# Performance work log

Hardware: AMD Instinct MI355X
Metric: run time of the kernel (lower is better)

Reference implementation:

```python
import jax, jax.numpy as jnp
import numpy as np

H = 16
W = 16
THRESH = 1.0
B = 32

# NOTE: [5.0, 1.0] reproduces the (likely buggy) constant in the original source.
SRC_POINTS = jnp.array([[0.0,0.0],[0.5,0.0],[1.0,0.0],[0.0,0.5],[0.5,0.5],[1.0,0.5],[0.0,1.0],[5.0,1.0],[1.0,1.0]], dtype=jnp.float32)

def _conv(x, w, stride, padding):
    return jax.lax.conv_general_dilated(x, w, (stride, stride), padding, dimension_numbers=('NHWC', 'HWIO', 'NHWC'))

def _tps_u(r):
    return r * r * jnp.log(r + 1e-6)

def _pdist(a, b):
    # a [...,2], b [n,2] -> [..., n] euclidean distances (eps for sqrt-at-0 safety)
    return jnp.sqrt(jnp.sum((a[..., None, :] - b) ** 2, axis=-1) + 1e-12)

def _tps_fit(ctrl, values):
    # cheind/py-thin-plate-spline TPS.fit with reduced=True. ctrl [n,2], values [n] -> theta [n+2]
    n = ctrl.shape[0]
    K = _tps_u(_pdist(ctrl, ctrl))
    P = jnp.concatenate([jnp.ones((n, 1), ctrl.dtype), ctrl], axis=1)
    A = jnp.zeros((n + 3, n + 3), ctrl.dtype)
    A = A.at[:n, :n].set(K).at[:n, n:].set(P).at[n:, :n].set(P.T)
    v = jnp.zeros(n + 3, ctrl.dtype).at[:n].set(values)
    theta = jnp.linalg.solve(A, v)
    return theta[1:]

def _tps_z(pts, ctrl, theta):
    # pts [m,2], theta reduced [n+2] -> [m]
    U = _tps_u(_pdist(pts, ctrl))
    w, a = theta[:-3], theta[-3:]
    w = jnp.concatenate([-jnp.sum(w, keepdims=True), w])
    return U @ w + a[0] + pts[:, 0] * a[1] + pts[:, 1] * a[2]

def _inlier_mask(geo):
    # geo [18] -> mask [H, W, H, W], mask[a_y, a_x, b_y, b_x]
    mv = geo.reshape(9, 2)
    dst = SRC_POINTS + mv
    delta = SRC_POINTS - dst  # c_src - c_dst (tps_theta_from_points)
    th_x = _tps_fit(dst, delta[:, 0])
    th_y = _tps_fit(dst, delta[:, 1])
    xs = jnp.linspace(0.0, 1.0, W)
    ys = jnp.linspace(0.0, 1.0, H)
    gx, gy = jnp.meshgrid(xs, ys)  # [H, W], gx varies along b_x
    pts = jnp.stack([gx.ravel(), gy.ravel()], axis=-1)
    ax = (gx + _tps_z(pts, dst, th_x).reshape(H, W)) * (H - 1)  # grid[...,0]*(map_size[0]-1)
    ay = (gy + _tps_z(pts, dst, th_y).reshape(H, W)) * (W - 1)
    # integer x in [ceil(ax-t), floor(ax+t)] clipped to [0,W-1]  <=>  |x - ax| <= t for x in range
    ix = jnp.arange(W, dtype=ax.dtype)
    iy = jnp.arange(H, dtype=ay.dtype)
    mx = jnp.abs(ix[:, None, None] - ax[None]) <= THRESH  # [W(a_x), H(b_y), W(b_x)]
    my = jnp.abs(iy[:, None, None] - ay[None]) <= THRESH  # [H(a_y), H(b_y), W(b_x)]
    return (my[:, None] & mx[None]).astype(jnp.float32)   # [H, W, H, W]

def _forward(image_A, image_B, W1, W2, W3, W4, Wr1, Wr2, Wd, bd):
    def feat(img):
        x = jax.nn.relu(_conv(img, W1, 2, 'SAME'))   # 256 -> 128
        x = jax.nn.relu(_conv(x, W2, 2, 'SAME'))     # 128 -> 64
        x = jax.nn.relu(_conv(x, W3, 2, 'SAME'))     # 64 -> 32
        x = jax.nn.relu(_conv(x, W4, 2, 'SAME'))     # 32 -> 16
        return x / (jnp.linalg.norm(x, axis=-1, keepdims=True) + 1e-6)  # channelwise l2 norm
    fA = feat(image_A)
    fB = feat(image_B)
    corr = jnp.einsum('bijc,bklc->bijkl', fA, fB)    # [B, H, W, H, W]
    b = corr.shape[0]
    r = corr.reshape(b, H, W, H * W)
    r = jax.nn.relu(_conv(r, Wr1, 1, 'VALID'))       # 16 -> 10
    r = jax.nn.relu(_conv(r, Wr2, 1, 'VALID'))       # 10 -> 6
    geo = r.reshape(b, -1) @ Wd + bd                 # [B, 18]
    # tf.numpy_function blocks gradients -> stop_gradient on the mask path
    masks = jax.lax.stop_gradient(jax.vmap(_inlier_mask)(geo))
    return jnp.sum(corr * masks, axis=(1, 2, 3, 4))  # [B]

def setup_inputs():
    key = jax.random.key(0)
    ks = jax.random.split(key, 10)
    s = 0.05
    return {
        'image_A': jax.random.normal(ks[0], (B, 256, 256, 3), jnp.float32),
        'image_B': jax.random.normal(ks[1], (B, 256, 256, 3), jnp.float32),
        'W1': jax.random.normal(ks[2], (3, 3, 3, 64), jnp.float32) * s,
        'W2': jax.random.normal(ks[3], (3, 3, 64, 128), jnp.float32) * s,
        'W3': jax.random.normal(ks[4], (3, 3, 128, 256), jnp.float32) * s,
        'W4': jax.random.normal(ks[5], (3, 3, 256, 512), jnp.float32) * s,
        'Wr1': jax.random.normal(ks[6], (7, 7, 256, 128), jnp.float32) * s,
        'Wr2': jax.random.normal(ks[7], (5, 5, 128, 64), jnp.float32) * s,
        'Wd': jax.random.normal(ks[8], (2304, 18), jnp.float32) * s,
        'bd': jnp.zeros((18,), jnp.float32),
    }

def reference(image_A, image_B, W1, W2, W3, W4, Wr1, Wr2, Wd, bd):
    return _forward(image_A, image_B, W1, W2, W3, W4, Wr1, Wr2, Wd, bd)
```

## Files before the change

kernel.cpp:

```cpp
#include <hip/hip_runtime.h>
#include <math.h>


typedef __attribute__((ext_vector_type(8))) _Float16 f16x8;
typedef __attribute__((ext_vector_type(4))) _Float16 f16x4;
typedef __attribute__((ext_vector_type(4))) float f32x4;

__device__ __forceinline__ unsigned short f2h(float f) {
  return __builtin_bit_cast(unsigned short, (_Float16)f);
}

__device__ __forceinline__ void gl16(const unsigned short* g, _Float16* l) {
  auto* gp = (const __attribute__((address_space(1))) unsigned int*)(g);
  auto* lp = (__attribute__((address_space(3))) unsigned int*)(l);
  __builtin_amdgcn_global_load_lds(gp, lp, 16, 0, 0);
}

__global__ __launch_bounds__(256) void prep_all(
    const float* __restrict__ W1, const float* __restrict__ W2,
    const float* __restrict__ W3, const float* __restrict__ W4,
    const float* __restrict__ Wr1, const float* __restrict__ Wr2,
    unsigned short* __restrict__ WT1, unsigned short* __restrict__ WT2,
    unsigned short* __restrict__ WT3, unsigned short* __restrict__ WT4,
    unsigned short* __restrict__ WTr1, unsigned short* __restrict__ WTr2,
    float* __restrict__ ZPf) {
  long idx = (long)blockIdx.x * 256 + threadIdx.x;
  if (idx < 1024) { ZPf[idx] = 0.f; return; }
  idx -= 1024;
  if (idx < 2048) {
    const int o = (int)idx >> 5, k = (int)idx & 31;
    WT1[idx] = (k < 27) ? f2h(W1[(size_t)k * 64 + o]) : (unsigned short)0;
    return;
  }
  idx -= 2048;
  if (idx < 73728) {
    const int k = (int)idx / 128, o = (int)idx % 128;
    WT2[(size_t)o * 576 + k] = f2h(W2[idx]);
    return;
  }
  idx -= 73728;
  if (idx < 294912) {
    const int k = (int)idx / 256, o = (int)idx % 256;
    WT3[(size_t)o * 1152 + k] = f2h(W3[idx]);
    return;
  }
  idx -= 294912;
  if (idx < 1179648) {
    const int k = (int)idx / 512, o = (int)idx % 512;
    WT4[(size_t)o * 2304 + k] = f2h(W4[idx]);
    return;
  }
  idx -= 1179648;
  if (idx < 1605632) {
    const int k = (int)idx / 128, o = (int)idx % 128;
    WTr1[(size_t)o * 12544 + k] = f2h(Wr1[idx]);
    return;
  }
  idx -= 1605632;
  if (idx < 204800) {
    const int k = (int)idx / 64, o = (int)idx % 64;
    WTr2[(size_t)o * 3200 + k] = f2h(Wr2[idx]);
  }
}

__global__ __launch_bounds__(256) void conv1_mfma(const float* __restrict__ inA,
                                                  const float* __restrict__ inB,
                                                  const unsigned short* __restrict__ wt1,
                                                  unsigned short* __restrict__ out) {
  const int i = blockIdx.x;
  const int b = blockIdx.y;
  const int tid = threadIdx.x;
  const int lane = tid & 63, wid = tid >> 6;
  const int lrow = lane & 15, quad = lane >> 4;

  __shared__ _Float16 Rows[3][776];
  __shared__ _Float16 OutB[8192];

  const float* __restrict__ img = (b < 32) ? inA : inB;
  const float* __restrict__ inb = img + (size_t)(b & 31) * 196608;
  const f16x4 z4 = {0, 0, 0, 0};
#pragma unroll
  for (int di = 0; di < 3; ++di) {
    const int y = 2 * i + di;
    if (tid < 192) {
      f16x4 h4 = z4;
      if (y < 256) {
        const float4 v4 = *(const float4*)(inb + (size_t)y * 768 + tid * 4);
        h4[0] = (_Float16)v4.x; h4[1] = (_Float16)v4.y;
        h4[2] = (_Float16)v4.z; h4[3] = (_Float16)v4.w;
      }
      *(f16x4*)&Rows[di][tid * 4] = h4;
    }
    if (tid < 3) Rows[di][768 + tid] = (_Float16)0.f;
  }
  __syncthreads();

  f16x8 bf[4];
#pragma unroll
  for (int ni = 0; ni < 4; ++ni)
    bf[ni] = *(const f16x8*)(wt1 + (ni * 16 + lrow) * 32 + quad * 8);

  f16x8 af[2];
#pragma unroll
  for (int mi = 0; mi < 2; ++mi) {
    const int j = wid * 32 + mi * 16 + lrow;
#pragma unroll
    for (int s = 0; s < 8; ++s) {
      const int k = quad * 8 + s;
      if (k < 27) {
        const int di = k / 9, dj = (k / 3) % 3, c = k % 3;
        af[mi][s] = Rows[di][(2 * j + dj) * 3 + c];
      } else {
        af[mi][s] = (_Float16)0.f;
      }
    }
  }

  f32x4 acc[2][4];
#pragma unroll
  for (int mi = 0; mi < 2; ++mi)
#pragma unroll
    for (int ni = 0; ni < 4; ++ni) {
      const f32x4 z = {0.f, 0.f, 0.f, 0.f};
      acc[mi][ni] = __builtin_amdgcn_mfma_f32_16x16x32_f16(af[mi], bf[ni], z, 0, 0, 0);
    }

#pragma unroll
  for (int mi = 0; mi < 2; ++mi)
#pragma unroll
    for (int ni = 0; ni < 4; ++ni)
#pragma unroll
      for (int r = 0; r < 4; ++r) {
        const int j = wid * 32 + mi * 16 + quad * 4 + r;
        const int ch = ni * 16 + lrow;
        OutB[j * 64 + (ch ^ (((j >> 2) & 3) << 4))] =
            (_Float16)fmaxf(acc[mi][ni][r], 0.f);
      }
  __syncthreads();

  unsigned short* __restrict__ ob = out + (((size_t)b * 128 + i) * 128) * 64;
#pragma unroll
  for (int q2 = 0; q2 < 4; ++q2) {
    const int v = tid + 256 * q2;
    const int j = v >> 3, c0 = (v & 7) * 8;
    const f16x8 pack = *(const f16x8*)&OutB[j * 64 + (c0 ^ (((j >> 2) & 3) << 4))];
    *(f16x8*)&ob[(size_t)j * 64 + c0] = pack;
  }
}

template <int BM, int BN, int CIN, int COUT, int KH, int KW, int STRIDE,
          int SAMEPAD, int SPLIT, int SK, int BATB, int OUTF32, int RELU>
__global__ __launch_bounds__(256) void tile_conv(
    const unsigned short* __restrict__ in, const unsigned short* __restrict__ wt,
    unsigned short* __restrict__ outh, float* __restrict__ outf,
    const unsigned short* __restrict__ zp,
    int Hin, int Win, int Hout, int Wout, int aLo, int bLo) {
  constexpr int CPT = CIN / 32;
  constexpr int LA = BM / 64;
  constexpr int LB = BN / 64;
  constexpr int KTOT = KH * KW * CIN;
  constexpr int MT = BM / 32;
  constexpr int NT = BN / 32;
  constexpr int PL = 1 + SPLIT;
  constexpr int LPS = PL * (LA + LB);
  constexpr int ASTR = PL * BM * 32;
  constexpr int BSTR = PL * BN * 32;
  constexpr unsigned WCN =
      (unsigned)((LPS & 0xF) | (0x7 << 4) | (0xF << 8) | ((LPS >> 4) << 14));
  constexpr unsigned WC0 = (unsigned)((0x7 << 4) | (0xF << 8));
  __shared__ _Float16 SH[3 * (ASTR + BSTR)];
  static_assert(SK > 1 || (size_t)BM * BN <= (size_t)3 * (ASTR + BSTR),
                "bounce must fit in SH");

  const int t = threadIdx.x;
  const int lane = t & 63, wid = t >> 6;
  const int lrow = lane & 15, quad = lane >> 4;
  const int m0 = blockIdx.x * BM;
  const int n0 = blockIdx.y * BN;

  const int q8 = ((t & 3) ^ ((t >> 3) & 3)) * 8;

  int pixB[LA], iS[LA], jS[LA];
#pragma unroll
  for (int i = 0; i < LA; ++i) {
    const int r = (t >> 2) + 64 * i;
    const int m = m0 + r;
    const int j = m % Wout;
    const int t2 = m / Wout;
    const int ii = t2 % Hout;
    const int b = t2 / Hout;
    iS[i] = ii * STRIDE;
    jS[i] = j * STRIDE;
    pixB[i] = ((b * Hin + iS[i]) * Win + jS[i]) * CIN + q8;
  }
  const unsigned short* wb = wt;
  if (BATB) wb += (size_t)(m0 / (Hout * Wout)) * COUT * KTOT;
  int bofB[LB];
#pragma unroll
  for (int i = 0; i < LB; ++i) {
    const int r = (t >> 2) + 64 * i;
    bofB[i] = (n0 + r) * KTOT + q8;
  }

  f32x4 acc[MT][NT];
#pragma unroll
  for (int mi = 0; mi < MT; ++mi)
#pragma unroll
    for (int ni = 0; ni < NT; ++ni) acc[mi][ni] = {0.f, 0.f, 0.f, 0.f};

  const int mB = (wid >> 1) * (BM / 2);
  const int nB = (wid & 1) * (BN / 2);

  int offA[MT], offB[NT];
#pragma unroll
  for (int mi = 0; mi < MT; ++mi) {
    const int row = mB + mi * 16 + lrow;
    offA[mi] = row * 32 + ((quad ^ ((row >> 1) & 3)) * 8);
  }
#pragma unroll
  for (int ni = 0; ni < NT; ++ni) {
    const int row = nB + ni * 16 + lrow;
    offB[ni] = row * 32 + ((quad ^ ((row >> 1) & 3)) * 8);
  }

  int tap_lo = 0, tap_hi = KH * KW;
  if (SK > 1) {
    tap_lo = (int)blockIdx.z * KH * KW / SK;
    tap_hi = ((int)blockIdx.z + 1) * KH * KW / SK;
  }
  const int ch_lo = tap_lo * CPT, ch_hi = tap_hi * CPT;

  auto stage = [&](int buf, int ch) {
    const int tap = ch / CPT;
    const int c0 = (ch & (CPT - 1)) * 32;
    const int di = tap / KW, dj = tap % KW;
    const int toff = (di * Win + dj) * CIN + c0;
    const int woff = tap * CIN + c0;
    _Float16* aB = SH + buf * ASTR;
    _Float16* bB = SH + 3 * ASTR + buf * BSTR;
#pragma unroll
    for (int i = 0; i < LA; ++i) {
      const bool ok = !SAMEPAD || ((iS[i] + di < Hin) && (jS[i] + dj < Win));
      const unsigned short* s0 = ok ? in + pixB[i] + toff : zp + q8;
      gl16(s0, aB + t * 8 + 2048 * i);
      if (SPLIT) {
        const unsigned short* s1 = ok ? in + pixB[i] + toff + aLo : zp + q8;
        gl16(s1, aB + BM * 32 + t * 8 + 2048 * i);
      }
    }
#pragma unroll
    for (int i = 0; i < LB; ++i) {
      gl16(wb + bofB[i] + woff, bB + t * 8 + 2048 * i);
      if (SPLIT)
        gl16(wb + bofB[i] + woff + bLo, bB + BN * 32 + t * 8 + 2048 * i);
    }
  };

  stage(0, ch_lo);
  if (ch_lo + 1 < ch_hi) stage(1, ch_lo + 1);
  int cur = 0;
  for (int ch = ch_lo; ch < ch_hi; ++ch) {
    if (ch + 1 < ch_hi) __builtin_amdgcn_s_waitcnt(WCN);
    else __builtin_amdgcn_s_waitcnt(WC0);
    __builtin_amdgcn_sched_barrier(0);
    __builtin_amdgcn_s_barrier();
    __builtin_amdgcn_sched_barrier(0);
    if (ch + 2 < ch_hi) stage(cur == 0 ? 2 : cur - 1, ch + 2);
    {
      const _Float16* aB = SH + cur * ASTR;
      const _Float16* bB = SH + 3 * ASTR + cur * BSTR;
      f16x8 af[MT], bf[NT], al[MT], bl[NT];
#pragma unroll
      for (int mi = 0; mi < MT; ++mi) {
        af[mi] = *(const f16x8*)&aB[offA[mi]];
        if (SPLIT) al[mi] = *(const f16x8*)&aB[BM * 32 + offA[mi]];
      }
#pragma unroll
      for (int ni = 0; ni < NT; ++ni) {
        bf[ni] = *(const f16x8*)&bB[offB[ni]];
        if (SPLIT) bl[ni] = *(const f16x8*)&bB[BN * 32 + offB[ni]];
      }
#pragma unroll
      for (int mi = 0; mi < MT; ++mi)
#pragma unroll
        for (int ni = 0; ni < NT; ++ni) {
          if (SPLIT) {
            acc[mi][ni] = __builtin_amdgcn_mfma_f32_16x16x32_f16(af[mi], bl[ni],
                                                                 acc[mi][ni], 0, 0, 0);
            acc[mi][ni] = __builtin_amdgcn_mfma_f32_16x16x32_f16(al[mi], bf[ni],
                                                                 acc[mi][ni], 0, 0, 0);
          }
          acc[mi][ni] = __builtin_amdgcn_mfma_f32_16x16x32_f16(af[mi], bf[ni],
                                                               acc[mi][ni], 0, 0, 0);
        }
    }
    cur = (cur == 2) ? 0 : cur + 1;
  }

  if (SK > 1) {
    const size_t slice = (size_t)blockIdx.z * ((size_t)gridDim.x * BM * COUT);
#pragma unroll
    for (int mi = 0; mi < MT; ++mi)
#pragma unroll
      for (int ni = 0; ni < NT; ++ni)
#pragma unroll
        for (int r = 0; r < 4; ++r) {
          const int row = m0 + mB + mi * 16 + quad * 4 + r;
          const int col = n0 + nB + ni * 16 + lrow;
          outf[slice + (size_t)row * COUT + col] = acc[mi][ni][r];
        }
  } else {
    __syncthreads();
    _Float16* bounce = &SH[0];
#pragma unroll
    for (int mi = 0; mi < MT; ++mi)
#pragma unroll
      for (int ni = 0; ni < NT; ++ni)
#pragma unroll
        for (int r = 0; r < 4; ++r) {
          const int row = mB + mi * 16 + quad * 4 + r;
          const int col = nB + ni * 16 + lrow;
          float v = acc[mi][ni][r];
          if (OUTF32) {
            outf[(size_t)(m0 + row) * COUT + n0 + col] = v;
          } else if (RELU) {
            v = fmaxf(v, 0.f);
          }
          bounce[row * BN + (col ^ (((row >> 2) & 3) << 4))] = (_Float16)v;
        }
    __syncthreads();
    constexpr int VPT = (BM * BN / 8) / 256;
#pragma unroll
    for (int q2 = 0; q2 < VPT; ++q2) {
      const int v = t + 256 * q2;
      const int rowL = v / (BN / 8);
      const int c0 = (v % (BN / 8)) * 8;
      const f16x8 pack =
          *(const f16x8*)&bounce[rowL * BN + (c0 ^ (((rowL >> 2) & 3) << 4))];
      *(f16x8*)&outh[(size_t)(m0 + rowL) * COUT + n0 + c0] = pack;
    }
  }
}

template <int MT, int NT, int CIN, int COUT, int KH, int KW, int SK>
__global__ __launch_bounds__(256) void gemm_conv(
    const unsigned short* __restrict__ in, const unsigned short* __restrict__ wt,
    float* __restrict__ outf, int Hin, int Win, int Hout, int Wout) {
  const int KTOT = KH * KW * CIN;
  const int lane = threadIdx.x & 63;
  const int wid = threadIdx.x >> 6;
  const int lrow = lane & 15;
  const int quad = lane >> 4;
  const int m0 = (blockIdx.x * 4 + wid) * (16 * MT);
  const int n0 = blockIdx.y * (16 * NT);

  int pix[MT];
#pragma unroll
  for (int mi = 0; mi < MT; ++mi) {
    const int m = m0 + mi * 16 + lrow;
    const int j = m % Wout;
    const int t = m / Wout;
    const int i = t % Hout;
    const int b = t / Hout;
    pix[mi] = (b * Hin + i) * Win + j;
  }
  const unsigned short* brow[NT];
#pragma unroll
  for (int ni = 0; ni < NT; ++ni)
    brow[ni] = wt + (size_t)(n0 + ni * 16 + lrow) * KTOT + quad * 8;

  f32x4 acc[MT][NT];
#pragma unroll
  for (int mi = 0; mi < MT; ++mi)
#pragma unroll
    for (int ni = 0; ni < NT; ++ni) acc[mi][ni] = {0.f, 0.f, 0.f, 0.f};

  const int tap_lo = (int)blockIdx.z * KH * KW / SK;
  const int tap_hi = ((int)blockIdx.z + 1) * KH * KW / SK;
  for (int tap = tap_lo; tap < tap_hi; ++tap) {
    const int di = tap / KW, dj = tap % KW;
    const unsigned short* ap[MT];
#pragma unroll
    for (int mi = 0; mi < MT; ++mi)
      ap[mi] = in + ((size_t)pix[mi] + di * Win + dj) * CIN + quad * 8;
    const int ko = tap * CIN;
#pragma unroll
    for (int c0 = 0; c0 < CIN; c0 += 32) {
      f16x8 ah[MT], bh[NT];
#pragma unroll
      for (int mi = 0; mi < MT; ++mi) ah[mi] = *(const f16x8*)(ap[mi] + c0);
#pragma unroll
      for (int ni = 0; ni < NT; ++ni) bh[ni] = *(const f16x8*)(brow[ni] + ko + c0);
#pragma unroll
      for (int mi = 0; mi < MT; ++mi)
#pragma unroll
        for (int ni = 0; ni < NT; ++ni)
          acc[mi][ni] = __builtin_amdgcn_mfma_f32_16x16x32_f16(ah[mi], bh[ni],
                                                               acc[mi][ni], 0, 0, 0);
    }
  }
  const size_t slice = (size_t)blockIdx.z * ((size_t)gridDim.x * 64 * MT * COUT);
#pragma unroll
  for (int mi = 0; mi < MT; ++mi)
#pragma unroll
    for (int ni = 0; ni < NT; ++ni)
#pragma unroll
      for (int r = 0; r < 4; ++r) {
        const int row = m0 + mi * 16 + quad * 4 + r;
        const int col = n0 + ni * 16 + lrow;
        outf[slice + (size_t)row * COUT + col] = acc[mi][ni][r];
      }
}

__global__ __launch_bounds__(256) void sum_relu_s(const float* __restrict__ p,
                                                  unsigned short* __restrict__ o,
                                                  int n, int parts) {
  const int idx = blockIdx.x * 256 + threadIdx.x;
  if (idx < n) {
    float v = 0.f;
    for (int s = 0; s < parts; ++s) v += p[(size_t)s * n + idx];
    o[idx] = f2h(fmaxf(v, 0.f));
  }
}
__global__ __launch_bounds__(256) void sum_relu_f(const float* __restrict__ p,
                                                  float* __restrict__ o,
                                                  int n, int parts) {
  const int idx = blockIdx.x * 256 + threadIdx.x;
  if (idx < n) {
    float v = 0.f;
    for (int s = 0; s < parts; ++s) v += p[(size_t)s * n + idx];
    o[idx] = fmaxf(v, 0.f);
  }
}

__global__ __launch_bounds__(64) void l2norm_k(const unsigned short* __restrict__ x,
                                               unsigned short* __restrict__ y,
                                               int loOff) {
  const int lane = threadIdx.x;
  const f16x8 v = *(const f16x8*)(x + (size_t)blockIdx.x * 512 + lane * 8);
  float f[8];
  float s = 0.f;
#pragma unroll
  for (int k = 0; k < 8; ++k) {
    f[k] = (float)v[k];
    s += f[k] * f[k];
  }
#pragma unroll
  for (int off = 32; off; off >>= 1) s += __shfl_xor(s, off, 64);
  const float inv = 1.f / (sqrtf(s) + 1e-6f);
  f16x8 vh, vl;
#pragma unroll
  for (int k = 0; k < 8; ++k) {
    const float nv = f[k] * inv;
    const _Float16 hi = (_Float16)nv;
    vh[k] = hi;
    vl[k] = (_Float16)(nv - (float)hi);
  }
  unsigned short* ph = y + (size_t)blockIdx.x * 512 + lane * 8;
  *(f16x8*)ph = vh;
  *(f16x8*)(ph + (size_t)loOff) = vl;
}

__global__ __launch_bounds__(64) void dense_k(const float* __restrict__ r2,
                                              const float* __restrict__ wd,
                                              const float* __restrict__ bd,
                                              float* __restrict__ geo) {
  const int o = blockIdx.x;
  const int b = blockIdx.y;
  const int lane = threadIdx.x;
  const float* __restrict__ rb = r2 + (size_t)b * 2304;
  float s = 0.f;
  for (int k = lane; k < 2304; k += 64) s += rb[k] * wd[(size_t)k * 18 + o];
#pragma unroll
  for (int off = 32; off; off >>= 1) s += __shfl_xor(s, off, 64);
  if (lane == 0) geo[b * 18 + o] = s + bd[o];
}

__device__ __forceinline__ float tps_u(float r) { return r * r * logf(r + 1e-6f); }

__global__ __launch_bounds__(64) void tps_k(const float* __restrict__ geo,
                                            float* __restrict__ axb,
                                            float* __restrict__ ayb) {
  const int b = blockIdx.x;
  const int tid = threadIdx.x;
  __shared__ float M[12][14];
  __shared__ float fel[12];
  __shared__ float dxs[9], dys[9];
  __shared__ float th[2][12];
  __shared__ float sW[2][9];
  __shared__ float sA[2][3];
  __shared__ int sPiv;

  const float srcx[9] = {0.f, 0.5f, 1.f, 0.f, 0.5f, 1.f, 0.f, 5.f, 1.f};
  const float srcy[9] = {0.f, 0.f, 0.f, 0.5f, 0.5f, 0.5f, 1.f, 1.f, 1.f};

  if (tid < 9) {
    const float mx = geo[b * 18 + 2 * tid], my = geo[b * 18 + 2 * tid + 1];
    dxs[tid] = srcx[tid] + mx;
    dys[tid] = srcy[tid] + my;
    M[tid][12] = -mx;
    M[tid][13] = -my;
  } else if (tid < 12) {
    M[tid][12] = 0.f;
    M[tid][13] = 0.f;
  }
  __syncthreads();
  for (int e = tid; e < 81; e += 64) {
    const int p = e / 9, q = e % 9;
    const float ddx = dxs[p] - dxs[q], ddy = dys[p] - dys[q];
    const float r = sqrtf(ddx * ddx + ddy * ddy + 1e-12f);
    M[p][q] = tps_u(r);
  }
  if (tid < 9) {
    M[tid][9] = 1.f;  M[tid][10] = dxs[tid]; M[tid][11] = dys[tid];
    M[9][tid] = 1.f;  M[10][tid] = dxs[tid]; M[11][tid] = dys[tid];
  } else if (tid < 12) {
    M[tid][9] = 0.f; M[tid][10] = 0.f; M[tid][11] = 0.f;
  }
  __syncthreads();

  for (int k = 0; k < 12; ++k) {
    if (tid == 0) {
      int piv = k;
      float best = fabsf(M[k][k]);
      for (int r = k + 1; r < 12; ++r) {
        const float v = fabsf(M[r][k]);
        if (v > best) { best = v; piv = r; }
      }
      sPiv = piv;
    }
    __syncthreads();
    const int piv = sPiv;
    if (piv != k && tid < 14) {
      const float tmp = M[k][tid];
      M[k][tid] = M[piv][tid];
      M[piv][tid] = tmp;
    }
    __syncthreads();
    if (tid > k && tid < 12) fel[tid] = M[tid][k] / M[k][k];
    __syncthreads();
    for (int e = tid; e < (11 - k) * 14; e += 64) {
      const int r = k + 1 + e / 14, cc = e % 14;
      if (cc >= k) M[r][cc] -= fel[r] * M[k][cc];
    }
    __syncthreads();
  }

  const int grp = tid >> 4;
  const int cc = tid & 15;
  for (int k = 11; k >= 0; --k) {
    float prod = 0.f;
    if (grp < 2 && cc > k && cc < 12) prod = M[k][cc] * th[grp][cc];
#pragma unroll
    for (int off = 8; off; off >>= 1) prod += __shfl_xor(prod, off, 16);
    if (grp < 2 && cc == 0) th[grp][k] = (M[k][12 + grp] - prod) / M[k][k];
    __syncthreads();
  }

  if (tid < 2) {
    float sw = 0.f;
    for (int p = 1; p < 9; ++p) {
      sW[tid][p] = th[tid][p];
      sw += th[tid][p];
    }
    sW[tid][0] = -sw;
    sA[tid][0] = th[tid][9];
    sA[tid][1] = th[tid][10];
    sA[tid][2] = th[tid][11];
  }
  __syncthreads();

  for (int p = tid; p < 256; p += 64) {
    const int pi = p >> 4, pj = p & 15;
    const float x = pj * (1.f / 15.f), y = pi * (1.f / 15.f);
    float zx = sA[0][0] + x * sA[0][1] + y * sA[0][2];
    float zy = sA[1][0] + x * sA[1][1] + y * sA[1][2];
#pragma unroll
    for (int c = 0; c < 9; ++c) {
      const float ddx = x - dxs[c], ddy = y - dys[c];
      const float r = sqrtf(ddx * ddx + ddy * ddy + 1e-12f);
      const float u = tps_u(r);
      zx += u * sW[0][c];
      zy += u * sW[1][c];
    }
    axb[b * 256 + p] = (x + zx) * 15.f;
    ayb[b * 256 + p] = (y + zy) * 15.f;
  }
}

__global__ __launch_bounds__(256) void masksum_k(const float* __restrict__ corr,
                                                 const float* __restrict__ axb,
                                                 const float* __restrict__ ayb,
                                                 float* __restrict__ out) {
  const int b = blockIdx.x;
  const int pB = threadIdx.x;
  const float ax = axb[b * 256 + pB];
  const float ay = ayb[b * 256 + pB];
  const float* __restrict__ cb = corr + (size_t)b * 65536;
  float s = 0.f;
  for (int i = 0; i < 16; ++i) {
    if (fabsf((float)i - ay) <= 1.0f) {
      const float* __restrict__ ci = cb + (size_t)i * 16 * 256 + pB;
      for (int j = 0; j < 16; ++j) {
        if (fabsf((float)j - ax) <= 1.0f) s += ci[(size_t)j * 256];
      }
    }
  }
  __shared__ float sm[256];
  sm[pB] = s;
  __syncthreads();
  for (int off = 128; off; off >>= 1) {
    if (pB < off) sm[pB] += sm[pB + off];
    __syncthreads();
  }
  if (pB == 0) out[b] = sm[0];
}

extern "C" void kernel_launch(void* const* d_in, const int* in_sizes, int n_in,
                              void* d_out, int out_size, void* d_ws, size_t ws_size,
                              hipStream_t stream) {
  const float* imgA = (const float*)d_in[0];
  const float* imgB = (const float*)d_in[1];
  const float* W1 = (const float*)d_in[2];
  const float* W2 = (const float*)d_in[3];
  const float* W3 = (const float*)d_in[4];
  const float* W4 = (const float*)d_in[5];
  const float* Wr1 = (const float*)d_in[6];
  const float* Wr2 = (const float*)d_in[7];
  const float* Wd = (const float*)d_in[8];
  const float* bd = (const float*)d_in[9];

  float* ws = (float*)d_ws;
  unsigned short* WT2 = (unsigned short*)(ws + 0);
  unsigned short* WT3 = (unsigned short*)(ws + 36864);
  unsigned short* WT4 = (unsigned short*)(ws + 184320);
  unsigned short* WTr1 = (unsigned short*)(ws + 774144);
  unsigned short* WTr2 = (unsigned short*)(ws + 1576960);
  unsigned short* FEATs = (unsigned short*)(ws + 1679360);
  unsigned short* S3both = (unsigned short*)(ws + 5873664);
  unsigned short* S2both = (unsigned short*)(ws + 14262272);
  unsigned short* S1both = (unsigned short*)(ws + 31039488);
  unsigned short* FEATsp = (unsigned short*)(ws + 5873664);
  float* CORRf = ws + 14262272;
  unsigned short* CORRh = (unsigned short*)(ws + 16359424);
  float* R1p = ws + 17408000;
  unsigned short* R1h = (unsigned short*)(ws + 27648000);
  float* R2p = ws + 27750400;
  float* R2f = ws + 29593600;
  float* GEOb = ws + 29667328;
  float* AXb = ws + 29667904;
  float* AYb = ws + 29676096;
  unsigned short* WT1 = (unsigned short*)(ws + 64593920);
  float* ZPf = ws + 64594944;
  const unsigned short* ZP = (const unsigned short*)ZPf;

  prep_all<<<13132, 256, 0, stream>>>(W1, W2, W3, W4, Wr1, Wr2,
                                      WT1, WT2, WT3, WT4, WTr1, WTr2, ZPf);

  conv1_mfma<<<dim3(128, 64), 256, 0, stream>>>(imgA, imgB, WT1, S1both);
  tile_conv<128, 128, 64, 128, 3, 3, 2, 1, 0, 1, 0, 0, 1>
      <<<dim3(2048, 1), 256, 0, stream>>>(S1both, WT2, S2both, nullptr, ZP,
                                          128, 128, 64, 64, 0, 0);
  tile_conv<128, 128, 128, 256, 3, 3, 2, 1, 0, 1, 0, 0, 1>
      <<<dim3(512, 2), 256, 0, stream>>>(S2both, WT3, S3both, nullptr, ZP,
                                         64, 64, 32, 32, 0, 0);
  tile_conv<128, 128, 256, 512, 3, 3, 2, 1, 0, 1, 0, 0, 1>
      <<<dim3(128, 4), 256, 0, stream>>>(S3both, WT4, FEATs, nullptr, ZP,
                                         32, 32, 16, 16, 0, 0);

  l2norm_k<<<16384, 64, 0, stream>>>(FEATs, FEATsp, 8388608);
  tile_conv<64, 64, 512, 256, 1, 1, 1, 0, 1, 1, 1, 1, 0>
      <<<dim3(128, 4), 256, 0, stream>>>(FEATsp, FEATsp + 4194304, CORRh, CORRf,
                                         ZP, 16, 16, 16, 16, 8388608, 8388608);
  tile_conv<128, 128, 256, 128, 7, 7, 1, 0, 0, 25, 0, 0, 0>
      <<<dim3(25, 1, 25), 256, 0, stream>>>(CORRh, WTr1, nullptr, R1p, ZP,
                                            16, 16, 10, 10, 0, 0);
  sum_relu_s<<<1600, 256, 0, stream>>>(R1p, R1h, 409600, 25);
  gemm_conv<1, 4, 128, 64, 5, 5, 25>
      <<<dim3(18, 1, 25), 256, 0, stream>>>(R1h, WTr2, R2p, 10, 10, 6, 6);
  sum_relu_f<<<288, 256, 0, stream>>>(R2p, R2f, 73728, 25);
  dense_k<<<dim3(18, 32), 64, 0, stream>>>(R2f, Wd, bd, GEOb);
  tps_k<<<32, 64, 0, stream>>>(GEOb, AXb, AYb);
  masksum_k<<<32, 256, 0, stream>>>(CORRf, AXb, AYb, (float*)d_out);
}
```

Baseline: 417.5 us.

## Add double-buffered 64-channel-step conv kernel for conv2 and conv3 layers

Adds a new tile_conv_db kernel variant and renames the existing one to tile_conv_r3. The new kernel stages 64 input channels per step into two LDS buffers with an XOR swizzle, where the old one used 32 channels across three rotating buffers. It does two MFMA k-substeps per barrier pair, with the aim of halving the number of barriers and waits per K element for the conv2 and conv3 layers. The trade-off is a shallower prefetch depth and a larger LDS footprint per stage, which could reduce occupancy or hide global-load latency less well.

Result: no change. 412.1 us (-1.3%).

```diff
diff --git a/kernel.cpp b/kernel.cpp
--- a/kernel.cpp
+++ b/kernel.cpp
@@ -150,7 +150,191 @@
 
 template <int BM, int BN, int CIN, int COUT, int KH, int KW, int STRIDE,
           int SAMEPAD, int SPLIT, int SK, int BATB, int OUTF32, int RELU>
-__global__ __launch_bounds__(256) void tile_conv(
+__global__ __launch_bounds__(256) void tile_conv_db(
+    const unsigned short* __restrict__ in, const unsigned short* __restrict__ wt,
+    unsigned short* __restrict__ outh, float* __restrict__ outf,
+    const unsigned short* __restrict__ zp,
+    int Hin, int Win, int Hout, int Wout, int aLo, int bLo) {
+  constexpr int CPT = CIN / 64;
+  constexpr int LA = BM / 32;
+  constexpr int LB = BN / 32;
+  constexpr int KTOT = KH * KW * CIN;
+  constexpr int MT = BM / 32;
+  constexpr int NT = BN / 32;
+  constexpr int PL = 1 + SPLIT;
+  constexpr int LPS = PL * (LA + LB);
+  constexpr unsigned WCN =
+      (unsigned)((LPS & 0xF) | (0x7 << 4) | (0xF << 8) | ((LPS >> 4) << 14));
+  constexpr unsigned WC0 = (unsigned)((0x7 << 4) | (0xF << 8));
+  __shared__ _Float16 As[2][PL * BM * 64];
+  __shared__ _Float16 Bs[2][PL * BN * 64];
+  static_assert(SK > 1 || (size_t)BM * BN <= sizeof(As) / sizeof(_Float16),
+                "bounce must fit in As");
+
+  const int t = threadIdx.x;
+  const int lane = t & 63, wid = t >> 6;
+  const int lrow = lane & 15, quad = lane >> 4;
+  const int m0 = blockIdx.x * BM;
+  const int n0 = blockIdx.y * BN;
+
+  const int q8 = ((t & 7) ^ ((t >> 3) & 7)) * 8;
+
+  int pixB[LA], iS[LA], jS[LA];
+#pragma unroll
+  for (int i = 0; i < LA; ++i) {
+    const int r = (t >> 3) + 32 * i;
+    const int m = m0 + r;
+    const int j = m % Wout;
+    const int t2 = m / Wout;
+    const int ii = t2 % Hout;
+    const int b = t2 / Hout;
+    iS[i] = ii * STRIDE;
+    jS[i] = j * STRIDE;
+    pixB[i] = ((b * Hin + iS[i]) * Win + jS[i]) * CIN + q8;
+  }
+  const unsigned short* wb = wt;
+  if (BATB) wb += (size_t)(m0 / (Hout * Wout)) * COUT * KTOT;
+  int bofB[LB];
+#pragma unroll
+  for (int i = 0; i < LB; ++i) {
+    const int r = (t >> 3) + 32 * i;
+    bofB[i] = (n0 + r) * KTOT + q8;
+  }
+
+  f32x4 acc[MT][NT];
+#pragma unroll
+  for (int mi = 0; mi < MT; ++mi)
+#pragma unroll
+    for (int ni = 0; ni < NT; ++ni) acc[mi][ni] = {0.f, 0.f, 0.f, 0.f};
+
+  const int mB = (wid >> 1) * (BM / 2);
+  const int nB = (wid & 1) * (BN / 2);
+
+  int tap_lo = 0, tap_hi = KH * KW;
+  if (SK > 1) {
+    tap_lo = (int)blockIdx.z * KH * KW / SK;
+    tap_hi = ((int)blockIdx.z + 1) * KH * KW / SK;
+  }
+  const int ch_lo = tap_lo * CPT, ch_hi = tap_hi * CPT;
+
+  auto stage = [&](int buf, int ch) {
+    const int tap = ch / CPT;
+    const int c0 = (ch % CPT) * 64;
+    const int di = tap / KW, dj = tap % KW;
+    const int toff = (di * Win + dj) * CIN + c0;
+    const int woff = tap * CIN + c0;
+#pragma unroll
+    for (int i = 0; i < LA; ++i) {
+      const bool ok = !SAMEPAD || ((iS[i] + di < Hin) && (jS[i] + dj < Win));
+      const unsigned short* s0 = ok ? in + pixB[i] + toff : zp + q8;
+      gl16(s0, &As[buf][t * 8 + 2048 * i]);
+      if (SPLIT) {
+        const unsigned short* s1 = ok ? in + pixB[i] + toff + aLo : zp + q8;
+        gl16(s1, &As[buf][BM * 64 + t * 8 + 2048 * i]);
+      }
+    }
+#pragma unroll
+    for (int i = 0; i < LB; ++i) {
+      gl16(wb + bofB[i] + woff, &Bs[buf][t * 8 + 2048 * i]);
+      if (SPLIT)
+        gl16(wb + bofB[i] + woff + bLo, &Bs[buf][BN * 64 + t * 8 + 2048 * i]);
+    }
+  };
+
+  stage(0, ch_lo);
+  if (ch_lo + 1 < ch_hi) stage(1, ch_lo + 1);
+  int cur = 0;
+  for (int ch = ch_lo; ch < ch_hi; ++ch) {
+    if (ch + 1 < ch_hi) __builtin_amdgcn_s_waitcnt(WCN);
+    else __builtin_amdgcn_s_waitcnt(WC0);
+    __builtin_amdgcn_sched_barrier(0);
+    __builtin_amdgcn_s_barrier();
+    __builtin_amdgcn_sched_barrier(0);
+#pragma unroll
+    for (int ks = 0; ks < 2; ++ks) {
+      f16x8 af[MT], bf[NT], al[MT], bl[NT];
+#pragma unroll
+      for (int mi = 0; mi < MT; ++mi) {
+        const int row = mB + mi * 16 + lrow;
+        const int off = row * 64 + (((ks * 4 + quad) ^ (row & 7)) * 8);
+        af[mi] = *(const f16x8*)&As[cur][off];
+        if (SPLIT) al[mi] = *(const f16x8*)&As[cur][BM * 64 + off];
+      }
+#pragma unroll
+      for (int ni = 0; ni < NT; ++ni) {
+        const int row = nB + ni * 16 + lrow;
+        const int off = row * 64 + (((ks * 4 + quad) ^ (row & 7)) * 8);
+        bf[ni] = *(const f16x8*)&Bs[cur][off];
+        if (SPLIT) bl[ni] = *(const f16x8*)&Bs[cur][BN * 64 + off];
+      }
+#pragma unroll
+      for (int mi = 0; mi < MT; ++mi)
+#pragma unroll
+        for (int ni = 0; ni < NT; ++ni) {
+          if (SPLIT) {
+            acc[mi][ni] = __builtin_amdgcn_mfma_f32_16x16x32_f16(af[mi], bl[ni],
+                                                                 acc[mi][ni], 0, 0, 0);
+            acc[mi][ni] = __builtin_amdgcn_mfma_f32_16x16x32_f16(al[mi], bf[ni],
+                                                                 acc[mi][ni], 0, 0, 0);
+          }
+          acc[mi][ni] = __builtin_amdgcn_mfma_f32_16x16x32_f16(af[mi], bf[ni],
+                                                               acc[mi][ni], 0, 0, 0);
+        }
+    }
+    __builtin_amdgcn_sched_barrier(0);
+    __builtin_amdgcn_s_barrier();
+    __builtin_amdgcn_sched_barrier(0);
+    if (ch + 2 < ch_hi) stage(cur, ch + 2);
+    cur ^= 1;
+  }
+
+  if (SK > 1) {
+    const size_t slice = (size_t)blockIdx.z * ((size_t)gridDim.x * BM * COUT);
+#pragma unroll
+    for (int mi = 0; mi < MT; ++mi)
+#pragma unroll
+      for (int ni = 0; ni < NT; ++ni)
+#pragma unroll
+        for (int r = 0; r < 4; ++r) {
+          const int row = m0 + mB + mi * 16 + quad * 4 + r;
+          const int col = n0 + nB + ni * 16 + lrow;
+          outf[slice + (size_t)row * COUT + col] = acc[mi][ni][r];
+        }
+  } else {
+    _Float16* bounce = &As[0][0];
+#pragma unroll
+    for (int mi = 0; mi < MT; ++mi)
+#pragma unroll
+      for (int ni = 0; ni < NT; ++ni)
+#pragma unroll
+        for (int r = 0; r < 4; ++r) {
+          const int row = mB + mi * 16 + quad * 4 + r;
+          const int col = nB + ni * 16 + lrow;
+          float v = acc[mi][ni][r];
+          if (OUTF32) {
+            outf[(size_t)(m0 + row) * COUT + n0 + col] = v;
+          } else if (RELU) {
+            v = fmaxf(v, 0.f);
+          }
+          bounce[row * BN + (col ^ (((row >> 2) & 3) << 4))] = (_Float16)v;
+        }
+    __syncthreads();
+    constexpr int VPT = (BM * BN / 8) / 256;
+#pragma unroll
+    for (int q2 = 0; q2 < VPT; ++q2) {
+      const int v = t + 256 * q2;
+      const int rowL = v / (BN / 8);
+      const int c0 = (v % (BN / 8)) * 8;
+      const f16x8 pack =
+          *(const f16x8*)&bounce[rowL * BN + (c0 ^ (((rowL >> 2) & 3) << 4))];
+      *(f16x8*)&outh[(size_t)(m0 + rowL) * COUT + n0 + c0] = pack;
+    }
+  }
+}
+
+template <int BM, int BN, int CIN, int COUT, int KH, int KW, int STRIDE,
+          int SAMEPAD, int SPLIT, int SK, int BATB, int OUTF32, int RELU>
+__global__ __launch_bounds__(256) void tile_conv_r3(
     const unsigned short* __restrict__ in, const unsigned short* __restrict__ wt,
     unsigned short* __restrict__ outh, float* __restrict__ outf,
     const unsigned short* __restrict__ zp,
@@ -658,21 +842,21 @@
                                       WT1, WT2, WT3, WT4, WTr1, WTr2, ZPf);
 
   conv1_mfma<<<dim3(128, 64), 256, 0, stream>>>(imgA, imgB, WT1, S1both);
-  tile_conv<128, 128, 64, 128, 3, 3, 2, 1, 0, 1, 0, 0, 1>
+  tile_conv_db<128, 128, 64, 128, 3, 3, 2, 1, 0, 1, 0, 0, 1>
       <<<dim3(2048, 1), 256, 0, stream>>>(S1both, WT2, S2both, nullptr, ZP,
                                           128, 128, 64, 64, 0, 0);
-  tile_conv<128, 128, 128, 256, 3, 3, 2, 1, 0, 1, 0, 0, 1>
+  tile_conv_db<128, 128, 128, 256, 3, 3, 2, 1, 0, 1, 0, 0, 1>
       <<<dim3(512, 2), 256, 0, stream>>>(S2both, WT3, S3both, nullptr, ZP,
                                          64, 64, 32, 32, 0, 0);
-  tile_conv<128, 128, 256, 512, 3, 3, 2, 1, 0, 1, 0, 0, 1>
+  tile_conv_r3<128, 128, 256, 512, 3, 3, 2, 1, 0, 1, 0, 0, 1>
       <<<dim3(128, 4), 256, 0, stream>>>(S3both, WT4, FEATs, nullptr, ZP,
                                          32, 32, 16, 16, 0, 0);
 
   l2norm_k<<<16384, 64, 0, stream>>>(FEATs, FEATsp, 8388608);
-  tile_conv<64, 64, 512, 256, 1, 1, 1, 0, 1, 1, 1, 1, 0>
+  tile_conv_r3<64, 64, 512, 256, 1, 1, 1, 0, 1, 1, 1, 1, 0>
       <<<dim3(128, 4), 256, 0, stream>>>(FEATsp, FEATsp + 4194304, CORRh, CORRf,
                                          ZP, 16, 16, 16, 16, 8388608, 8388608);
-  tile_conv<128, 128, 256, 128, 7, 7, 1, 0, 0, 25, 0, 0, 0>
+  tile_conv_r3<128, 128, 256, 128, 7, 7, 1, 0, 0, 25, 0, 0, 0>
       <<<dim3(25, 1, 25), 256, 0, stream>>>(CORRh, WTr1, nullptr, R1p, ZP,
                                             16, 16, 10, 10, 0, 0);
   sum_relu_s<<<1600, 256, 0, stream>>>(R1p, R1h, 409600, 25);
```
